# Optimization experiments

Hardware: AMD Instinct MI355X
Metric: run time of the kernel (lower is better)

The kernel has to match this reference:

```python
import jax, jax.numpy as jnp
import numpy as np

B, H, W, C = 32, 512, 512, 3


def dct2_matrix(N):
    # Orthonormal DCT-II basis: D[k, n] = s_k * sqrt(2/N) * cos(pi*(2n+1)*k/(2N))
    n = np.arange(N)
    k = n[:, None]
    D = np.cos(np.pi * (2 * n[None, :] + 1) * k / (2.0 * N)) * np.sqrt(2.0 / N)
    D[0, :] *= 1.0 / np.sqrt(2.0)  # ortho scaling of DC row
    return jnp.asarray(D, dtype=jnp.float32)


def setup_inputs() -> dict:
    key = jax.random.key(0)
    x = jax.random.normal(key, (B, H, W, C), dtype=jnp.float32)
    return {"x": x}


def reference(x) -> jnp.ndarray:
    # 2D DCT-II (ortho) along height and width, channels untouched.
    Dh = dct2_matrix(x.shape[1])  # [H, H]
    Dw = dct2_matrix(x.shape[2])  # [W, W]
    y = jnp.einsum('kh,bhwc->bkwc', Dh, x)   # DCT over height
    y = jnp.einsum('lw,bkwc->bklc', Dw, y)   # DCT over width
    return y
```

## Files before the change

kernel.cpp:

```cpp
#include <hip/hip_runtime.h>
#include <stdint.h>


typedef __bf16 bf16_t;
typedef bf16_t bf16x8 __attribute__((ext_vector_type(8)));
typedef float  f32x4  __attribute__((ext_vector_type(4)));

__device__ __forceinline__ uint32_t f2bf(float f) {
    union { float f; uint32_t u; } v; v.f = f;
    uint32_t r = v.u + 0x7fffu + ((v.u >> 16) & 1u);
    return r >> 16;
}

__device__ __forceinline__ f32x4 mfma16(bf16x8 a, bf16x8 b, f32x4 c) {
    return __builtin_amdgcn_mfma_f32_16x16x32_bf16(a, b, c, 0, 0, 0);
}

__device__ __forceinline__ void load_lds16(const void* g, void* l) {
    __builtin_amdgcn_global_load_lds(
        (const __attribute__((address_space(1))) uint32_t*)g,
        (__attribute__((address_space(3))) uint32_t*)l, 16, 0, 0);
}

__global__ __launch_bounds__(256) void gen_dct(uint16_t* __restrict__ Dbf) {
    int idx = blockIdx.x * 256 + threadIdx.x;
    int k = idx >> 9, h = idx & 511;
    int phase = ((2 * h + 1) * k) & 2047;
    float ang = (float)phase * 3.0679615757712823e-3f;
    float s = (k == 0) ? 0.04419417382415922f : 0.0625f;
    Dbf[idx] = (uint16_t)f2bf(__cosf(ang) * s);
}

__global__ __launch_bounds__(256, 3) void pass1(const float* __restrict__ x,
                                                const uint16_t* __restrict__ Dbf,
                                                uint16_t* __restrict__ Y) {
    __shared__ __align__(16) uint16_t Alds[128 * 32];
    __shared__ __align__(16) uint16_t Blds[96 * 32];
    const int t = threadIdx.x;
    const int lane = t & 63, wv = t >> 6;
    const int nt = blockIdx.x;
    const int mt = blockIdx.y;
    const int b  = blockIdx.z;
    const float* xb = x + (size_t)b * (512 * 1536);

    const int jl = t % 96;
    const int hh = t / 96;
    const int wl = jl / 3, cc = jl - 3 * wl;
    const int ncol = cc * 32 + ((wl >> 1) + ((wl & 1) << 4));
    const int xv = (ncol >> 1) & 3;
    const int jg = nt * 96 + jl;

    f32x4 acc[2][6] = {};

    for (int kt = 0; kt < 16; ++kt) {
        __syncthreads();
        {
            int q = t;
            load_lds16(Dbf + (size_t)(mt * 128 + (q >> 2)) * 512 + kt * 32 + (q & 3) * 8,
                       Alds + q * 8);
            int q2 = t + 256;
            load_lds16(Dbf + (size_t)(mt * 128 + (q2 >> 2)) * 512 + kt * 32 + (q2 & 3) * 8,
                       Alds + q2 * 8);
        }
        if (t < 192) {
            const float* src = xb + (size_t)(kt * 32 + hh * 16) * 1536 + jg;
            float v[16];
#pragma unroll
            for (int r = 0; r < 16; ++r) v[r] = src[(size_t)r * 1536];
            uint32_t p[8];
#pragma unroll
            for (int i = 0; i < 8; ++i)
                p[i] = f2bf(v[2 * i]) | (f2bf(v[2 * i + 1]) << 16);
            *(uint4*)&Blds[ncol * 32 + (((hh * 2 + 0) ^ xv) << 3)] =
                make_uint4(p[0], p[1], p[2], p[3]);
            *(uint4*)&Blds[ncol * 32 + (((hh * 2 + 1) ^ xv) << 3)] =
                make_uint4(p[4], p[5], p[6], p[7]);
        }
        __syncthreads();

        bf16x8 aq[2];
#pragma unroll
        for (int i = 0; i < 2; ++i)
            aq[i] = *(bf16x8*)&Alds[((wv * 2 + i) * 16 + (lane & 15)) * 32 + ((lane >> 4) << 3)];
#pragma unroll
        for (int tt = 0; tt < 6; ++tt) {
            int col = tt * 16 + (lane & 15);
            bf16x8 bq = *(bf16x8*)&Blds[col * 32 + (((lane >> 4) ^ ((col >> 1) & 3)) << 3)];
            acc[0][tt] = mfma16(aq[0], bq, acc[0][tt]);
            acc[1][tt] = mfma16(aq[1], bq, acc[1][tt]);
        }
    }

    const int wg = nt * 32 + 2 * (lane & 15);
#pragma unroll
    for (int i = 0; i < 2; ++i) {
        int kg = mt * 128 + (wv * 2 + i) * 16 + ((lane >> 4) << 2);
#pragma unroll
        for (int c = 0; c < 3; ++c)
#pragma unroll
            for (int r = 0; r < 4; ++r) {
                uint32_t pk = f2bf(acc[i][2 * c][r]) | (f2bf(acc[i][2 * c + 1][r]) << 16);
                *(uint32_t*)&Y[(size_t)b * 786432 + (size_t)(kg + r) * 1536 + c * 512 + wg] = pk;
            }
    }
}

__global__ __launch_bounds__(256, 3) void pass2(const uint16_t* __restrict__ Y,
                                                const uint16_t* __restrict__ Dbf,
                                                float* __restrict__ out) {
    __shared__ __align__(16) char smem[96 * 130 * 4];
    uint16_t* Alds = (uint16_t*)smem;
    uint16_t* Blds = (uint16_t*)(smem + 6144);
    float*    Elds = (float*)smem;
    const int t = threadIdx.x;
    const int lane = t & 63, wv = t >> 6;
    const int lt = blockIdx.x;
    const int mt = blockIdx.y;
    const int b  = blockIdx.z;
    const size_t yb = (size_t)b * 786432;

    f32x4 acc[6][2] = {};

    for (int kt = 0; kt < 16; ++kt) {
        __syncthreads();
        {
            int q = t;
            load_lds16(Y + yb + (size_t)(mt * 96 + (q >> 2)) * 512 + kt * 32 + (q & 3) * 8,
                       Alds + q * 8);
            if (t < 128) {
                int q2 = 256 + t;
                load_lds16(Y + yb + (size_t)(mt * 96 + (q2 >> 2)) * 512 + kt * 32 + (q2 & 3) * 8,
                           Alds + q2 * 8);
            }
            int q3 = t;
            load_lds16(Dbf + (size_t)(lt * 128 + (q3 >> 2)) * 512 + kt * 32 + (q3 & 3) * 8,
                       Blds + q3 * 8);
            int q4 = t + 256;
            load_lds16(Dbf + (size_t)(lt * 128 + (q4 >> 2)) * 512 + kt * 32 + (q4 & 3) * 8,
                       Blds + q4 * 8);
        }
        __syncthreads();

        bf16x8 bq[2];
#pragma unroll
        for (int p = 0; p < 2; ++p)
            bq[p] = *(bf16x8*)&Blds[((wv * 2 + p) * 16 + (lane & 15)) * 32 + ((lane >> 4) << 3)];
#pragma unroll
        for (int tt = 0; tt < 6; ++tt) {
            bf16x8 aq = *(bf16x8*)&Alds[(tt * 16 + (lane & 15)) * 32 + ((lane >> 4) << 3)];
            acc[tt][0] = mfma16(aq, bq[0], acc[tt][0]);
            acc[tt][1] = mfma16(aq, bq[1], acc[tt][1]);
        }
    }

    __syncthreads();
#pragma unroll
    for (int tt = 0; tt < 6; ++tt)
#pragma unroll
        for (int p = 0; p < 2; ++p) {
            int m = tt * 16 + ((lane >> 4) << 2);
            int ll = (wv * 2 + p) * 16 + (lane & 15);
#pragma unroll
            for (int r = 0; r < 4; ++r)
                Elds[(m + r) * 130 + ll] = acc[tt][p][r];
        }
    __syncthreads();

    const int kloc = t >> 3, sub = t & 7;
    size_t ob = (size_t)b * 786432 + (size_t)(mt * 32 + kloc) * 1536 + lt * 384 + sub * 48;
#pragma unroll
    for (int q = 0; q < 12; ++q) {
        int o0 = sub * 48 + q * 4;
        float4 v;
        v.x = Elds[(kloc * 3 + ((o0 + 0) % 3)) * 130 + (o0 + 0) / 3];
        v.y = Elds[(kloc * 3 + ((o0 + 1) % 3)) * 130 + (o0 + 1) / 3];
        v.z = Elds[(kloc * 3 + ((o0 + 2) % 3)) * 130 + (o0 + 2) / 3];
        v.w = Elds[(kloc * 3 + ((o0 + 3) % 3)) * 130 + (o0 + 3) / 3];
        *(float4*)&out[ob + q * 4] = v;
    }
}

extern "C" void kernel_launch(void* const* d_in, const int* in_sizes, int n_in,
                              void* d_out, int out_size, void* d_ws, size_t ws_size,
                              hipStream_t stream) {
    (void)in_sizes; (void)n_in; (void)out_size; (void)ws_size;
    const float* x = (const float*)d_in[0];
    float* out = (float*)d_out;
    uint16_t* Dbf = (uint16_t*)d_ws;
    uint16_t* Y   = (uint16_t*)d_ws + 512 * 512;

    gen_dct<<<1024, 256, 0, stream>>>(Dbf);
    dim3 g1(16, 4, 32);
    pass1<<<g1, 256, 0, stream>>>(x, Dbf, Y);
    dim3 g2(4, 16, 32);
    pass2<<<g2, 256, 0, stream>>>(Y, Dbf, out);
}
```

Before: 292.2 us.

## Reorder DCT passes to width-first with coalesced row loads and register prefetch

Runs the width DCT first, reading contiguous rows of x as float4 vectors instead of strided per-column loads. The intermediate is stored in a transposed channel-major layout so the height pass can read it contiguously. The K-step grows to 64 with XOR-swizzled LDS tiles, the next tile is prefetched into registers while the MFMAs run, and occupancy is raised to 4 blocks. The cost is more complex index math and a larger LDS footprint, and the output epilogue is staged in two phases through LDS.

```diff
diff --git a/kernel.cpp b/kernel.cpp
--- a/kernel.cpp
+++ b/kernel.cpp
@@ -4,6 +4,7 @@
 
 typedef __bf16 bf16_t;
 typedef bf16_t bf16x8 __attribute__((ext_vector_type(8)));
+typedef bf16_t bf16x4 __attribute__((ext_vector_type(4)));
 typedef float  f32x4  __attribute__((ext_vector_type(4)));
 
 __device__ __forceinline__ uint32_t f2bf(float f) {
@@ -31,152 +32,191 @@
     Dbf[idx] = (uint16_t)f2bf(__cosf(ang) * s);
 }
 
-__global__ __launch_bounds__(256, 3) void pass1(const float* __restrict__ x,
-                                                const uint16_t* __restrict__ Dbf,
-                                                uint16_t* __restrict__ Y) {
-    __shared__ __align__(16) uint16_t Alds[128 * 32];
-    __shared__ __align__(16) uint16_t Blds[96 * 32];
-    const int t = threadIdx.x;
-    const int lane = t & 63, wv = t >> 6;
-    const int nt = blockIdx.x;
-    const int mt = blockIdx.y;
+__global__ __launch_bounds__(256, 4) void pass_w(const float* __restrict__ x,
+                                                 const uint16_t* __restrict__ Dbf,
+                                                 uint16_t* __restrict__ Y1) {
+    __shared__ __align__(16) uint16_t Ax[96 * 64];
+    __shared__ __align__(16) uint16_t Bd[128 * 64];
+    const int t = threadIdx.x, lane = t & 63, wv = t >> 6;
+    const int quad = lane >> 4, l15 = lane & 15;
+    const int lt = blockIdx.x;
+    const int ht = blockIdx.y;
     const int b  = blockIdx.z;
-    const float* xb = x + (size_t)b * (512 * 1536);
-
-    const int jl = t % 96;
-    const int hh = t / 96;
-    const int wl = jl / 3, cc = jl - 3 * wl;
-    const int ncol = cc * 32 + ((wl >> 1) + ((wl & 1) << 4));
-    const int xv = (ncol >> 1) & 3;
-    const int jg = nt * 96 + jl;
-
-    f32x4 acc[2][6] = {};
-
-    for (int kt = 0; kt < 16; ++kt) {
-        __syncthreads();
+
+    const int hl = t >> 3, wq = t & 7;
+    const float* xrow = x + (size_t)b * 786432 + (size_t)(ht * 32 + hl) * 1536 + wq * 24;
+
+    const uint16_t* srcD[4];
+#pragma unroll
+    for (int i = 0; i < 4; ++i) {
+        int p = i * 256 + t, row = p >> 3, jj = (p & 7) ^ (row & 7);
+        srcD[i] = Dbf + (size_t)(lt * 128 + row) * 512 + jj * 8;
+    }
+
+    float4 xr[6];
+#pragma unroll
+    for (int i = 0; i < 6; ++i) xr[i] = *(const float4*)(xrow + i * 4);
+
+    f32x4 acc[6][2] = {};
+
+    for (int kt = 0; kt < 8; ++kt) {
+        __syncthreads();
+#pragma unroll
+        for (int i = 0; i < 4; ++i)
+            load_lds16(srcD[i] + kt * 64, Bd + (i * 256 + t) * 8);
         {
-            int q = t;
-            load_lds16(Dbf + (size_t)(mt * 128 + (q >> 2)) * 512 + kt * 32 + (q & 3) * 8,
-                       Alds + q * 8);
-            int q2 = t + 256;
-            load_lds16(Dbf + (size_t)(mt * 128 + (q2 >> 2)) * 512 + kt * 32 + (q2 & 3) * 8,
-                       Alds + q2 * 8);
-        }
-        if (t < 192) {
-            const float* src = xb + (size_t)(kt * 32 + hh * 16) * 1536 + jg;
-            float v[16];
-#pragma unroll
-            for (int r = 0; r < 16; ++r) v[r] = src[(size_t)r * 1536];
-            uint32_t p[8];
-#pragma unroll
-            for (int i = 0; i < 8; ++i)
-                p[i] = f2bf(v[2 * i]) | (f2bf(v[2 * i + 1]) << 16);
-            *(uint4*)&Blds[ncol * 32 + (((hh * 2 + 0) ^ xv) << 3)] =
-                make_uint4(p[0], p[1], p[2], p[3]);
-            *(uint4*)&Blds[ncol * 32 + (((hh * 2 + 1) ^ xv) << 3)] =
-                make_uint4(p[4], p[5], p[6], p[7]);
-        }
-        __syncthreads();
-
-        bf16x8 aq[2];
-#pragma unroll
-        for (int i = 0; i < 2; ++i)
-            aq[i] = *(bf16x8*)&Alds[((wv * 2 + i) * 16 + (lane & 15)) * 32 + ((lane >> 4) << 3)];
-#pragma unroll
-        for (int tt = 0; tt < 6; ++tt) {
-            int col = tt * 16 + (lane & 15);
-            bf16x8 bq = *(bf16x8*)&Blds[col * 32 + (((lane >> 4) ^ ((col >> 1) & 3)) << 3)];
-            acc[0][tt] = mfma16(aq[0], bq, acc[0][tt]);
-            acc[1][tt] = mfma16(aq[1], bq, acc[1][tt]);
-        }
-    }
-
-    const int wg = nt * 32 + 2 * (lane & 15);
-#pragma unroll
-    for (int i = 0; i < 2; ++i) {
-        int kg = mt * 128 + (wv * 2 + i) * 16 + ((lane >> 4) << 2);
-#pragma unroll
-        for (int c = 0; c < 3; ++c)
-#pragma unroll
-            for (int r = 0; r < 4; ++r) {
-                uint32_t pk = f2bf(acc[i][2 * c][r]) | (f2bf(acc[i][2 * c + 1][r]) << 16);
-                *(uint32_t*)&Y[(size_t)b * 786432 + (size_t)(kg + r) * 1536 + c * 512 + wg] = pk;
-            }
-    }
-}
-
-__global__ __launch_bounds__(256, 3) void pass2(const uint16_t* __restrict__ Y,
-                                                const uint16_t* __restrict__ Dbf,
-                                                float* __restrict__ out) {
-    __shared__ __align__(16) char smem[96 * 130 * 4];
-    uint16_t* Alds = (uint16_t*)smem;
-    uint16_t* Blds = (uint16_t*)(smem + 6144);
-    float*    Elds = (float*)smem;
-    const int t = threadIdx.x;
-    const int lane = t & 63, wv = t >> 6;
-    const int lt = blockIdx.x;
-    const int mt = blockIdx.y;
+            const float* xf = (const float*)xr;
+            const int wsw = ((wq + (hl & 7)) & 7) * 8;
+#pragma unroll
+            for (int c = 0; c < 3; ++c) {
+                bf16x8 hv;
+#pragma unroll
+                for (int u = 0; u < 8; ++u) hv[u] = (bf16_t)xf[c + 3 * u];
+                *(bf16x8*)&Ax[(c * 32 + hl) * 64 + wsw] = hv;
+            }
+        }
+        __syncthreads();
+        if (kt < 7) {
+#pragma unroll
+            for (int i = 0; i < 6; ++i)
+                xr[i] = *(const float4*)(xrow + (kt + 1) * 192 + i * 4);
+        }
+#pragma unroll
+        for (int ks = 0; ks < 2; ++ks) {
+            bf16x8 aq[6], bq[2];
+#pragma unroll
+            for (int tt = 0; tt < 6; ++tt) {
+                int m = tt * 16 + l15;
+                int ws = ((ks * 4 + quad + (m & 7)) & 7) * 8;
+                aq[tt] = *(const bf16x8*)&Ax[m * 64 + ws];
+            }
+#pragma unroll
+            for (int p = 0; p < 2; ++p) {
+                int n = wv * 32 + p * 16 + l15;
+                int pos = n * 8 + ((ks * 4 + quad) ^ (n & 7));
+                bq[p] = *(const bf16x8*)&Bd[pos * 8];
+            }
+#pragma unroll
+            for (int tt = 0; tt < 6; ++tt)
+#pragma unroll
+                for (int p = 0; p < 2; ++p)
+                    acc[tt][p] = mfma16(aq[tt], bq[p], acc[tt][p]);
+        }
+    }
+
+#pragma unroll
+    for (int tt = 0; tt < 6; ++tt) {
+        const int c = tt >> 1;
+        const int hb = (tt & 1) * 16 + quad * 4;
+#pragma unroll
+        for (int p = 0; p < 2; ++p) {
+            int n = wv * 32 + p * 16 + l15;
+            bf16x4 pk;
+#pragma unroll
+            for (int r = 0; r < 4; ++r) pk[r] = (bf16_t)acc[tt][p][r];
+            *(bf16x4*)&Y1[(size_t)b * 786432 + (size_t)c * 262144 +
+                          (size_t)(lt * 128 + n) * 512 + ht * 32 + hb] = pk;
+        }
+    }
+}
+
+__global__ __launch_bounds__(256, 4) void pass_h(const uint16_t* __restrict__ Y1,
+                                                 const uint16_t* __restrict__ Dbf,
+                                                 float* __restrict__ out) {
+    __shared__ __align__(16) char smem[28672];
+    uint16_t* Ad = (uint16_t*)smem;
+    uint16_t* By = (uint16_t*)(smem + 16384);
+    float*    El = (float*)smem;
+    const int t = threadIdx.x, lane = t & 63, wv = t >> 6;
+    const int quad = lane >> 4, l15 = lane & 15;
+    const int ktile = blockIdx.x;
+    const int lt = blockIdx.y;
     const int b  = blockIdx.z;
-    const size_t yb = (size_t)b * 786432;
+    const int l0 = lt * 32;
+
+    const uint16_t* srcA[4];
+#pragma unroll
+    for (int i = 0; i < 4; ++i) {
+        int p = i * 256 + t, row = p >> 3, jj = (p & 7) ^ (row & 7);
+        srcA[i] = Dbf + (size_t)(ktile * 128 + row) * 512 + jj * 8;
+    }
+    const uint16_t* srcB[3];
+#pragma unroll
+    for (int i = 0; i < 3; ++i) {
+        int p = i * 256 + t, row = p >> 3, jj = (p & 7) ^ (row & 7);
+        srcB[i] = Y1 + (size_t)b * 786432 + (size_t)(row >> 5) * 262144 +
+                  (size_t)(l0 + (row & 31)) * 512 + jj * 8;
+    }
+
+    uint4 yr[3];
+#pragma unroll
+    for (int i = 0; i < 3; ++i) yr[i] = *(const uint4*)srcB[i];
 
     f32x4 acc[6][2] = {};
 
-    for (int kt = 0; kt < 16; ++kt) {
-        __syncthreads();
-        {
-            int q = t;
-            load_lds16(Y + yb + (size_t)(mt * 96 + (q >> 2)) * 512 + kt * 32 + (q & 3) * 8,
-                       Alds + q * 8);
-            if (t < 128) {
-                int q2 = 256 + t;
-                load_lds16(Y + yb + (size_t)(mt * 96 + (q2 >> 2)) * 512 + kt * 32 + (q2 & 3) * 8,
-                           Alds + q2 * 8);
-            }
-            int q3 = t;
-            load_lds16(Dbf + (size_t)(lt * 128 + (q3 >> 2)) * 512 + kt * 32 + (q3 & 3) * 8,
-                       Blds + q3 * 8);
-            int q4 = t + 256;
-            load_lds16(Dbf + (size_t)(lt * 128 + (q4 >> 2)) * 512 + kt * 32 + (q4 & 3) * 8,
-                       Blds + q4 * 8);
-        }
-        __syncthreads();
-
-        bf16x8 bq[2];
-#pragma unroll
-        for (int p = 0; p < 2; ++p)
-            bq[p] = *(bf16x8*)&Blds[((wv * 2 + p) * 16 + (lane & 15)) * 32 + ((lane >> 4) << 3)];
-#pragma unroll
-        for (int tt = 0; tt < 6; ++tt) {
-            bf16x8 aq = *(bf16x8*)&Alds[(tt * 16 + (lane & 15)) * 32 + ((lane >> 4) << 3)];
-            acc[tt][0] = mfma16(aq, bq[0], acc[tt][0]);
-            acc[tt][1] = mfma16(aq, bq[1], acc[tt][1]);
-        }
-    }
-
-    __syncthreads();
-#pragma unroll
-    for (int tt = 0; tt < 6; ++tt)
-#pragma unroll
-        for (int p = 0; p < 2; ++p) {
-            int m = tt * 16 + ((lane >> 4) << 2);
-            int ll = (wv * 2 + p) * 16 + (lane & 15);
-#pragma unroll
-            for (int r = 0; r < 4; ++r)
-                Elds[(m + r) * 130 + ll] = acc[tt][p][r];
-        }
-    __syncthreads();
-
-    const int kloc = t >> 3, sub = t & 7;
-    size_t ob = (size_t)b * 786432 + (size_t)(mt * 32 + kloc) * 1536 + lt * 384 + sub * 48;
-#pragma unroll
-    for (int q = 0; q < 12; ++q) {
-        int o0 = sub * 48 + q * 4;
-        float4 v;
-        v.x = Elds[(kloc * 3 + ((o0 + 0) % 3)) * 130 + (o0 + 0) / 3];
-        v.y = Elds[(kloc * 3 + ((o0 + 1) % 3)) * 130 + (o0 + 1) / 3];
-        v.z = Elds[(kloc * 3 + ((o0 + 2) % 3)) * 130 + (o0 + 2) / 3];
-        v.w = Elds[(kloc * 3 + ((o0 + 3) % 3)) * 130 + (o0 + 3) / 3];
-        *(float4*)&out[ob + q * 4] = v;
+    for (int kt = 0; kt < 8; ++kt) {
+        __syncthreads();
+#pragma unroll
+        for (int i = 0; i < 4; ++i)
+            load_lds16(srcA[i] + kt * 64, Ad + (i * 256 + t) * 8);
+#pragma unroll
+        for (int i = 0; i < 3; ++i)
+            *(uint4*)&By[(i * 256 + t) * 8] = yr[i];
+        __syncthreads();
+        if (kt < 7) {
+#pragma unroll
+            for (int i = 0; i < 3; ++i)
+                yr[i] = *(const uint4*)(srcB[i] + (kt + 1) * 64);
+        }
+#pragma unroll
+        for (int ks = 0; ks < 2; ++ks) {
+            bf16x8 aq[2], bq[6];
+#pragma unroll
+            for (int p = 0; p < 2; ++p) {
+                int m = wv * 32 + p * 16 + l15;
+                int pos = m * 8 + ((ks * 4 + quad) ^ (m & 7));
+                aq[p] = *(const bf16x8*)&Ad[pos * 8];
+            }
+#pragma unroll
+            for (int tt = 0; tt < 6; ++tt) {
+                int n = tt * 16 + l15;
+                int pos = n * 8 + ((ks * 4 + quad) ^ (n & 7));
+                bq[tt] = *(const bf16x8*)&By[pos * 8];
+            }
+#pragma unroll
+            for (int tt = 0; tt < 6; ++tt)
+#pragma unroll
+                for (int p = 0; p < 2; ++p)
+                    acc[tt][p] = mfma16(aq[p], bq[tt], acc[tt][p]);
+        }
+    }
+
+    const int sub = t & 3, krow = t >> 2;
+#pragma unroll
+    for (int ph = 0; ph < 2; ++ph) {
+        __syncthreads();
+        if ((wv >> 1) == ph) {
+#pragma unroll
+            for (int p = 0; p < 2; ++p) {
+                int idx2 = wv * 2 + p;
+                int kb = (idx2 & 3) * 16 + quad * 4;
+#pragma unroll
+                for (int tt = 0; tt < 6; ++tt) {
+                    int n = tt * 16 + l15;
+                    int col = (n & 31) * 3 + (n >> 5);
+#pragma unroll
+                    for (int r = 0; r < 4; ++r)
+                        El[(kb + r) * 100 + col] = acc[tt][p][r];
+                }
+            }
+        }
+        __syncthreads();
+        float* dst = out + (size_t)b * 786432 +
+                     (size_t)(ktile * 128 + ph * 64 + krow) * 1536 + lt * 96 + sub * 24;
+        const float* srcE = El + krow * 100 + sub * 24;
+#pragma unroll
+        for (int i = 0; i < 6; ++i)
+            *(float4*)(dst + i * 4) = *(const float4*)(srcE + i * 4);
     }
 }
 
@@ -187,11 +227,11 @@
     const float* x = (const float*)d_in[0];
     float* out = (float*)d_out;
     uint16_t* Dbf = (uint16_t*)d_ws;
-    uint16_t* Y   = (uint16_t*)d_ws + 512 * 512;
+    uint16_t* Y1  = (uint16_t*)d_ws + 512 * 512;
 
     gen_dct<<<1024, 256, 0, stream>>>(Dbf);
-    dim3 g1(16, 4, 32);
-    pass1<<<g1, 256, 0, stream>>>(x, Dbf, Y);
+    dim3 g1(4, 16, 32);
+    pass_w<<<g1, 256, 0, stream>>>(x, Dbf, Y1);
     dim3 g2(4, 16, 32);
-    pass2<<<g2, 256, 0, stream>>>(Y, Dbf, out);
-}
+    pass_h<<<g2, 256, 0, stream>>>(Y1, Dbf, out);
+}
```

Measured after the change: 303.2 us. 1.04x slower.
